# Kernel tuning notes

Hardware: AMD Instinct MI355X
Metric: run time of the kernel (lower is better)

The kernel has to match this reference:

```python
import jax, jax.numpy as jnp
import numpy as np

N_NODES = 50000
N_EDGES = 800000
IN_FEAT = 512
HEADS = 4
OUT_FEAT = 64


def setup_inputs() -> dict:
    key = jax.random.key(0)
    k1, k2, k3 = jax.random.split(key, 3)
    x = jax.random.normal(k1, (N_NODES, IN_FEAT), dtype=jnp.float32)
    # W corresponds to nn.Linear(in, heads*out, bias=False).weight: (H*F, in)
    W = jax.random.normal(k2, (HEADS * OUT_FEAT, IN_FEAT), dtype=jnp.float32) * (1.0 / np.sqrt(IN_FEAT))
    edge_index = jax.random.randint(k3, (2, N_EDGES), 0, N_NODES, dtype=jnp.int32)
    return {"x": x, "W": W, "edge_index": edge_index}


def reference(x, W, edge_index):
    # h = W(x) viewed as (N, H, F)
    n = x.shape[0]
    hf = W.shape[0]
    h = (x @ W.T).reshape(n, HEADS, hf // HEADS)
    src, dst = edge_index[0], edge_index[1]
    # scatter-mean of h[src] into dst buckets (single O(E) pass, replaces per-node loop)
    msg = h[src]                                             # (E, H, F)
    summed = jax.ops.segment_sum(msg, dst, num_segments=n)   # (N, H, F)
    cnt = jax.ops.segment_sum(jnp.ones((edge_index.shape[1],), h.dtype), dst, num_segments=n)
    mean = summed / jnp.maximum(cnt, 1.0)[:, None, None]
    # nodes with no in-edges keep their own transformed features
    out = jnp.where((cnt > 0)[:, None, None], mean, h)
    return out.reshape(n, hf)
```

## Files before the change

kernel.cpp:

```cpp
#include <hip/hip_runtime.h>
#include <hip/hip_bf16.h>

#define N_NODES 50000
#define N_EDGES 800000
#define IN_FEAT 512
#define HF 256
#define BM 128
#define BN 128
#define BK 64
#define LDT 64
#define CAP 64
#define GEMM_BLOCKS 782
#define FILL_BLOCKS 218

typedef short short8 __attribute__((ext_vector_type(8)));
typedef float f32x4 __attribute__((ext_vector_type(4)));

__device__ __forceinline__ unsigned short f2bf(float f) {
    union { float f; unsigned u; } c{f};
    unsigned r = c.u + 0x7FFFu + ((c.u >> 16) & 1u);
    return (unsigned short)(r >> 16);
}
__device__ __forceinline__ float bf2f(unsigned short b) {
    union { unsigned u; float f; } c;
    c.u = ((unsigned)b) << 16;
    return c.f;
}
__device__ __forceinline__ short8 pack8(const float4& a, const float4& b) {
    short8 v;
    v[0] = (short)f2bf(a.x); v[1] = (short)f2bf(a.y);
    v[2] = (short)f2bf(a.z); v[3] = (short)f2bf(a.w);
    v[4] = (short)f2bf(b.x); v[5] = (short)f2bf(b.y);
    v[6] = (short)f2bf(b.z); v[7] = (short)f2bf(b.w);
    return v;
}
__device__ __forceinline__ int swz(int row, int col8) {
    return row * LDT + (col8 ^ ((row & 7) << 3));
}

__global__ __launch_bounds__(256) void gemm_fill_kernel(const float* __restrict__ X,
                                                        const float* __restrict__ Wm,
                                                        unsigned short* __restrict__ H,
                                                        const int* __restrict__ ei,
                                                        int* __restrict__ cnt,
                                                        int* __restrict__ bucket) {
    if (blockIdx.x >= GEMM_BLOCKS) {
        const int cb = blockIdx.x - GEMM_BLOCKS;
        const int stride = FILL_BLOCKS * 256;
        for (int e = cb * 256 + threadIdx.x; e < N_EDGES; e += stride) {
            const int src = ei[e];
            const int dst = ei[N_EDGES + e];
            const int pos = atomicAdd(&cnt[dst], 1);
            if (pos < CAP) bucket[dst * CAP + pos] = src;
        }
        return;
    }

    __shared__ short As[BM * LDT];
    __shared__ short Bs[BN * LDT];

    const int t    = threadIdx.x;
    const int lane = t & 63;
    const int w    = t >> 6;
    const int wr   = w >> 1;
    const int wc   = w & 1;
    const int brow = (blockIdx.x >> 1) * BM;
    const int bcol = (blockIdx.x & 1) * BN;

    const int tr = t >> 3;
    const int tc = (t & 7) * 8;

    int arow[4];
#pragma unroll
    for (int r = 0; r < 4; ++r) {
        int a = brow + r * 32 + tr;
        arow[r] = (a >= N_NODES) ? (N_NODES - 1) : a;
    }

    f32x4 acc[4][4] = {};

    for (int kt = 0; kt < IN_FEAT; kt += BK) {
#pragma unroll
        for (int r = 0; r < 4; ++r) {
            const int row = r * 32 + tr;
            const float* ga = X + (size_t)arow[r] * IN_FEAT + kt + tc;
            const float4 a0 = *(const float4*)(ga);
            const float4 a1 = *(const float4*)(ga + 4);
            *(short8*)(&As[swz(row, tc)]) = pack8(a0, a1);
        }
#pragma unroll
        for (int r = 0; r < 4; ++r) {
            const int row = r * 32 + tr;
            const float* gb = Wm + (size_t)(bcol + row) * IN_FEAT + kt + tc;
            const float4 b0 = *(const float4*)(gb);
            const float4 b1 = *(const float4*)(gb + 4);
            *(short8*)(&Bs[swz(row, tc)]) = pack8(b0, b1);
        }
        __syncthreads();

#pragma unroll
        for (int ks = 0; ks < 2; ++ks) {
            const int koff = ks * 32 + (lane >> 4) * 8;
            short8 a[4], b[4];
#pragma unroll
            for (int m = 0; m < 4; ++m) {
                const int row = wr * 64 + m * 16 + (lane & 15);
                a[m] = *(const short8*)(&As[swz(row, koff)]);
            }
#pragma unroll
            for (int n = 0; n < 4; ++n) {
                const int row = wc * 64 + n * 16 + (lane & 15);
                b[n] = *(const short8*)(&Bs[swz(row, koff)]);
            }
#pragma unroll
            for (int m = 0; m < 4; ++m)
#pragma unroll
                for (int n = 0; n < 4; ++n)
                    acc[m][n] = __builtin_amdgcn_mfma_f32_16x16x32_bf16(a[m], b[n], acc[m][n], 0, 0, 0);
        }
        __syncthreads();
    }

#pragma unroll
    for (int m = 0; m < 4; ++m) {
        const int row0 = brow + wr * 64 + m * 16 + (lane >> 4) * 4;
#pragma unroll
        for (int n = 0; n < 4; ++n) {
            const int col = bcol + wc * 64 + n * 16 + (lane & 15);
#pragma unroll
            for (int j = 0; j < 4; ++j) {
                const int row = row0 + j;
                if (row < N_NODES) H[(size_t)row * HF + col] = f2bf(acc[m][n][j]);
            }
        }
    }
}

__global__ __launch_bounds__(256) void aggregate_kernel(const unsigned short* __restrict__ h,
                                                        const int* __restrict__ cnt,
                                                        const int* __restrict__ bucket,
                                                        float* __restrict__ out) {
    const int node = (int)(((size_t)blockIdx.x * blockDim.x + threadIdx.x) >> 6);
    const int lane = threadIdx.x & 63;
    if (node >= N_NODES) return;
    int c = cnt[node];
    if (c > CAP) c = CAP;
    const int base = node * CAP;

    float a0 = 0.f, a1 = 0.f, a2 = 0.f, a3 = 0.f;

    int i = 0;
    for (; i + 4 <= c; i += 4) {
        const int s0 = bucket[base + i + 0];
        const int s1 = bucket[base + i + 1];
        const int s2 = bucket[base + i + 2];
        const int s3 = bucket[base + i + 3];
        const ushort4 v0 = *(const ushort4*)(h + (size_t)s0 * HF + lane * 4);
        const ushort4 v1 = *(const ushort4*)(h + (size_t)s1 * HF + lane * 4);
        const ushort4 v2 = *(const ushort4*)(h + (size_t)s2 * HF + lane * 4);
        const ushort4 v3 = *(const ushort4*)(h + (size_t)s3 * HF + lane * 4);
        a0 += bf2f(v0.x) + bf2f(v1.x) + bf2f(v2.x) + bf2f(v3.x);
        a1 += bf2f(v0.y) + bf2f(v1.y) + bf2f(v2.y) + bf2f(v3.y);
        a2 += bf2f(v0.z) + bf2f(v1.z) + bf2f(v2.z) + bf2f(v3.z);
        a3 += bf2f(v0.w) + bf2f(v1.w) + bf2f(v2.w) + bf2f(v3.w);
    }
    for (; i < c; ++i) {
        const int s0 = bucket[base + i];
        const ushort4 v0 = *(const ushort4*)(h + (size_t)s0 * HF + lane * 4);
        a0 += bf2f(v0.x); a1 += bf2f(v0.y); a2 += bf2f(v0.z); a3 += bf2f(v0.w);
    }

    float4 r;
    if (c > 0) {
        const float inv = 1.0f / (float)c;
        r.x = a0 * inv; r.y = a1 * inv; r.z = a2 * inv; r.w = a3 * inv;
    } else {
        const ushort4 v = *(const ushort4*)(h + (size_t)node * HF + lane * 4);
        r.x = bf2f(v.x); r.y = bf2f(v.y); r.z = bf2f(v.z); r.w = bf2f(v.w);
    }
    *(float4*)(out + (size_t)node * HF + lane * 4) = r;
}

extern "C" void kernel_launch(void* const* d_in, const int* in_sizes, int n_in,
                              void* d_out, int out_size, void* d_ws, size_t ws_size,
                              hipStream_t stream) {
    const float* x = (const float*)d_in[0];
    const float* W = (const float*)d_in[1];
    const int* ei  = (const int*)d_in[2];
    float* out = (float*)d_out;

    char* ws = (char*)d_ws;
    unsigned short* h = (unsigned short*)ws;
    int* bucket = (int*)(ws + (size_t)N_NODES * HF * 2);
    int* cnt    = (int*)((char*)bucket + (size_t)N_NODES * CAP * 4);

    hipMemsetAsync(cnt, 0, (size_t)N_NODES * sizeof(int), stream);

    gemm_fill_kernel<<<GEMM_BLOCKS + FILL_BLOCKS, 256, 0, stream>>>(x, W, h, ei, cnt, bucket);

    aggregate_kernel<<<(N_NODES * 64 + 255) / 256, 256, 0, stream>>>(h, cnt, bucket, out);
}
```

Before: 133.6 us.

## Load GEMM operands directly into MFMA registers and pre-convert W to bf16

Drops LDS staging and barriers from the GEMM. Each wave now loads its A fragments straight from global fp32 X and converts them in registers, and loads B fragments from a bf16 copy of W. A separate small kernel builds that bf16 W copy once per call. This removes the LDS traffic and __syncthreads, but each X row is now read by both column blocks and by several lanes per wave with less coalescing, and the loads are no longer reused through shared memory.

```diff
diff --git a/kernel.cpp b/kernel.cpp
--- a/kernel.cpp
+++ b/kernel.cpp
@@ -5,10 +5,6 @@
 #define N_EDGES 800000
 #define IN_FEAT 512
 #define HF 256
-#define BM 128
-#define BN 128
-#define BK 64
-#define LDT 64
 #define CAP 64
 #define GEMM_BLOCKS 782
 #define FILL_BLOCKS 218
@@ -34,12 +30,18 @@
     v[6] = (short)f2bf(b.z); v[7] = (short)f2bf(b.w);
     return v;
 }
-__device__ __forceinline__ int swz(int row, int col8) {
-    return row * LDT + (col8 ^ ((row & 7) << 3));
+
+__global__ __launch_bounds__(256) void convw_kernel(const float* __restrict__ Wm,
+                                                    unsigned short* __restrict__ Wb) {
+    const int i = (blockIdx.x * 256 + threadIdx.x) * 4;
+    const float4 v = *(const float4*)(Wm + i);
+    ushort4 o;
+    o.x = f2bf(v.x); o.y = f2bf(v.y); o.z = f2bf(v.z); o.w = f2bf(v.w);
+    *(ushort4*)(Wb + i) = o;
 }
 
 __global__ __launch_bounds__(256) void gemm_fill_kernel(const float* __restrict__ X,
-                                                        const float* __restrict__ Wm,
+                                                        const unsigned short* __restrict__ Wb,
                                                         unsigned short* __restrict__ H,
                                                         const int* __restrict__ ei,
                                                         int* __restrict__ cnt,
@@ -56,69 +58,46 @@
         return;
     }
 
-    __shared__ short As[BM * LDT];
-    __shared__ short Bs[BN * LDT];
-
     const int t    = threadIdx.x;
     const int lane = t & 63;
     const int w    = t >> 6;
     const int wr   = w >> 1;
     const int wc   = w & 1;
-    const int brow = (blockIdx.x >> 1) * BM;
-    const int bcol = (blockIdx.x & 1) * BN;
+    const int brow = (blockIdx.x >> 1) * 128;
+    const int bcol = (blockIdx.x & 1) * 128;
+    const int l15  = lane & 15;
+    const int lk   = (lane >> 4) * 8;
 
-    const int tr = t >> 3;
-    const int tc = (t & 7) * 8;
-
-    int arow[4];
+    const float* ap[4];
 #pragma unroll
-    for (int r = 0; r < 4; ++r) {
-        int a = brow + r * 32 + tr;
-        arow[r] = (a >= N_NODES) ? (N_NODES - 1) : a;
+    for (int m = 0; m < 4; ++m) {
+        int r = brow + wr * 64 + m * 16 + l15;
+        if (r >= N_NODES) r = N_NODES - 1;
+        ap[m] = X + (size_t)r * IN_FEAT + lk;
     }
+    const unsigned short* bp[4];
+#pragma unroll
+    for (int n = 0; n < 4; ++n)
+        bp[n] = Wb + (size_t)(bcol + wc * 64 + n * 16 + l15) * IN_FEAT + lk;
 
     f32x4 acc[4][4] = {};
 
-    for (int kt = 0; kt < IN_FEAT; kt += BK) {
+    for (int kt = 0; kt < IN_FEAT; kt += 32) {
+        short8 a[4], b[4];
 #pragma unroll
-        for (int r = 0; r < 4; ++r) {
-            const int row = r * 32 + tr;
-            const float* ga = X + (size_t)arow[r] * IN_FEAT + kt + tc;
-            const float4 a0 = *(const float4*)(ga);
-            const float4 a1 = *(const float4*)(ga + 4);
-            *(short8*)(&As[swz(row, tc)]) = pack8(a0, a1);
+        for (int m = 0; m < 4; ++m) {
+            const float4 x0 = *(const float4*)(ap[m] + kt);
+            const float4 x1 = *(const float4*)(ap[m] + kt + 4);
+            a[m] = pack8(x0, x1);
         }
 #pragma unroll
-        for (int r = 0; r < 4; ++r) {
-            const int row = r * 32 + tr;
-            const float* gb = Wm + (size_t)(bcol + row) * IN_FEAT + kt + tc;
-            const float4 b0 = *(const float4*)(gb);
-            const float4 b1 = *(const float4*)(gb + 4);
-            *(short8*)(&Bs[swz(row, tc)]) = pack8(b0, b1);
-        }
-        __syncthreads();
-
+        for (int n = 0; n < 4; ++n)
+            b[n] = *(const short8*)(bp[n] + kt);
 #pragma unroll
-        for (int ks = 0; ks < 2; ++ks) {
-            const int koff = ks * 32 + (lane >> 4) * 8;
-            short8 a[4], b[4];
+        for (int m = 0; m < 4; ++m)
 #pragma unroll
-            for (int m = 0; m < 4; ++m) {
-                const int row = wr * 64 + m * 16 + (lane & 15);
-                a[m] = *(const short8*)(&As[swz(row, koff)]);
-            }
-#pragma unroll
-            for (int n = 0; n < 4; ++n) {
-                const int row = wc * 64 + n * 16 + (lane & 15);
-                b[n] = *(const short8*)(&Bs[swz(row, koff)]);
-            }
-#pragma unroll
-            for (int m = 0; m < 4; ++m)
-#pragma unroll
-                for (int n = 0; n < 4; ++n)
-                    acc[m][n] = __builtin_amdgcn_mfma_f32_16x16x32_bf16(a[m], b[n], acc[m][n], 0, 0, 0);
-        }
-        __syncthreads();
+            for (int n = 0; n < 4; ++n)
+                acc[m][n] = __builtin_amdgcn_mfma_f32_16x16x32_bf16(a[m], b[n], acc[m][n], 0, 0, 0);
     }
 
 #pragma unroll
@@ -126,7 +105,7 @@
         const int row0 = brow + wr * 64 + m * 16 + (lane >> 4) * 4;
 #pragma unroll
         for (int n = 0; n < 4; ++n) {
-            const int col = bcol + wc * 64 + n * 16 + (lane & 15);
+            const int col = bcol + wc * 64 + n * 16 + l15;
 #pragma unroll
             for (int j = 0; j < 4; ++j) {
                 const int row = row0 + j;
@@ -190,13 +169,16 @@
     float* out = (float*)d_out;
 
     char* ws = (char*)d_ws;
-    unsigned short* h = (unsigned short*)ws;
+    unsigned short* h  = (unsigned short*)ws;
     int* bucket = (int*)(ws + (size_t)N_NODES * HF * 2);
     int* cnt    = (int*)((char*)bucket + (size_t)N_NODES * CAP * 4);
+    unsigned short* Wb = (unsigned short*)((char*)cnt + (size_t)N_NODES * 4);
 
     hipMemsetAsync(cnt, 0, (size_t)N_NODES * sizeof(int), stream);
 
-    gemm_fill_kernel<<<GEMM_BLOCKS + FILL_BLOCKS, 256, 0, stream>>>(x, W, h, ei, cnt, bucket);
+    convw_kernel<<<(HF * IN_FEAT) / (256 * 4), 256, 0, stream>>>(W, Wb);
+
+    gemm_fill_kernel<<<GEMM_BLOCKS + FILL_BLOCKS, 256, 0, stream>>>(x, Wb, h, ei, cnt, bucket);
 
     aggregate_kernel<<<(N_NODES * 64 + 255) / 256, 256, 0, stream>>>(h, cnt, bucket, out);
 }
```

Result: slower. 165.0 us (+23.5%).
